# Performance work log

Hardware: AMD Instinct MI355X
Metric: run time of the kernel (lower is better)

The kernel has to match this reference:

```python
import jax, jax.numpy as jnp
import numpy as np

INPUT, HIDDEN, OUTPUT, BATCH = 2048, 32, 512, 16384


def setup_inputs() -> dict:
    key = jax.random.key(0)
    k1, k2, k3, k4 = jax.random.split(key, 4)
    x = jax.random.normal(k1, (BATCH, INPUT), dtype=jnp.float32)
    # torch init: uniform(-1, 1) for both linear weights and hebbian coeffs
    w1 = jax.random.uniform(k2, (HIDDEN, INPUT), jnp.float32, -1.0, 1.0)
    w2 = jax.random.uniform(k3, (OUTPUT, HIDDEN), jnp.float32, -1.0, 1.0)
    heb_coeffs = jax.random.uniform(k4, (HIDDEN * INPUT + OUTPUT * HIDDEN, 4), jnp.float32, -1.0, 1.0)
    return {"x": x, "w1": w1, "w2": w2, "heb_coeffs": heb_coeffs}


def reference(x, w1, w2, heb_coeffs):
    # Forward MLP: act = relu(x @ w1^T), out = sigmoid(act @ w2^T) - 0.4
    act = jax.nn.relu(x @ w1.T)                 # [B, HIDDEN]
    out = jax.nn.sigmoid(act @ w2.T) - 0.4      # [B, OUTPUT]

    B = x.shape[0]
    # idx = (shape0-1)*i + i + j == shape0*i + j  -> coeff layout [in_dim, out_dim, 4]
    c1 = heb_coeffs[: HIDDEN * INPUT].reshape(INPUT, HIDDEN, 4)
    c2 = heb_coeffs[HIDDEN * INPUT :].reshape(HIDDEN, OUTPUT, 4)

    # ABCD update, batch loop -> batch-summed outer products / rank-1 terms
    corr1 = jnp.einsum("bi,bj->ij", x, act)     # [INPUT, HIDDEN]
    dw1T = (B * c1[..., 3]
            + c1[..., 0] * corr1
            + c1[..., 1] * x.sum(0)[:, None]
            + c1[..., 2] * act.sum(0)[None, :])  # [INPUT, HIDDEN]

    corr2 = jnp.einsum("bi,bj->ij", act, out)   # [HIDDEN, OUTPUT]
    dw2T = (B * c2[..., 3]
            + c2[..., 0] * corr2
            + c2[..., 1] * act.sum(0)[:, None]
            + c2[..., 2] * out.sum(0)[None, :])  # [HIDDEN, OUTPUT]

    w1_new = w1 + dw1T.T                        # [HIDDEN, INPUT]
    w2_new = w2 + dw2T.T                        # [OUTPUT, HIDDEN]
    # row-wise L2 normalization (torch.norm(dim=1, keepdim=True))
    w1_new = w1_new / jnp.linalg.norm(w1_new, axis=1, keepdims=True)
    w2_new = w2_new / jnp.linalg.norm(w2_new, axis=1, keepdims=True)
    return out, w1_new, w2_new
```

## Files before the change

### kernel.cpp

```cpp
#include <hip/hip_runtime.h>
#include <math.h>

constexpr int BATCH = 16384;
constexpr int IND   = 2048;
constexpr int HID   = 32;
constexpr int OUTD  = 512;

constexpr int NC1 = 64;
constexpr int NSA = 64;
constexpr int NC2 = 128;

constexpr int SA   = 136;
constexpr int SXT  = 72;
constexpr int SATW = 136;
constexpr int SAT2 = 264;

typedef __attribute__((ext_vector_type(8))) short bf16x8;
typedef __attribute__((ext_vector_type(4))) float f32x4;

__device__ __forceinline__ unsigned short f2bf(float f) {
  unsigned u = __float_as_uint(f);
  u += 0x7FFFu + ((u >> 16) & 1u);
  return (unsigned short)(u >> 16);
}
__device__ __forceinline__ float bf2f(unsigned short h) {
  return __uint_as_float(((unsigned)h) << 16);
}
__device__ __forceinline__ void split2(float f, unsigned short& hi,
                                       unsigned short& lo) {
  hi = f2bf(f);
  lo = f2bf(f - bf2f(hi));
}
__device__ __forceinline__ int swzA(int row, int col) {
  return row * SA + (col ^ (((row >> 3) & 7) * 8));
}

__global__ __launch_bounds__(256) void k_cvtw(
    const float* __restrict__ w1, const float* __restrict__ w2,
    unsigned short* __restrict__ w1H, unsigned short* __restrict__ w1L,
    unsigned short* __restrict__ w2H, unsigned short* __restrict__ w2L) {
  const int bid = blockIdx.x;
  if (bid < 64) {
    const int g = bid * 256 + threadIdx.x;
    float4 v = ((const float4*)w1)[g];
    ushort4 h, l;
    split2(v.x, h.x, l.x); split2(v.y, h.y, l.y);
    split2(v.z, h.z, l.z); split2(v.w, h.w, l.w);
    ((ushort4*)w1H)[g] = h;
    ((ushort4*)w1L)[g] = l;
  } else {
    const int g = (bid - 64) * 256 + threadIdx.x;
    float4 v = ((const float4*)w2)[g];
    ushort4 h, l;
    split2(v.x, h.x, l.x); split2(v.y, h.y, l.y);
    split2(v.z, h.z, l.z); split2(v.w, h.w, l.w);
    ((ushort4*)w2H)[g] = h;
    ((ushort4*)w2L)[g] = l;
  }
}

__global__ __launch_bounds__(256, 4) void k_act(
    const float* __restrict__ x, const unsigned short* __restrict__ w1H,
    const unsigned short* __restrict__ w1L, float* __restrict__ act_part,
    unsigned short* __restrict__ xH) {
  const int tid = threadIdx.x;
  const int kq = blockIdx.x & 1;
  const int bt = blockIdx.x >> 1;
  const int b0 = bt * 32;
  const int kbase = kq * 1024;
  const int lane = tid & 63;
  const int wv = tid >> 6;
  const int arow = lane & 15;
  const int m4 = lane >> 4;
  const int ksub = m4 * 8;
  const int rt = wv & 1;
  const int ht = wv >> 1;

  __shared__ __align__(16) unsigned short XH[32 * SA];
  __shared__ __align__(16) unsigned short XL[32 * SA];
  __shared__ __align__(16) unsigned short WH[32 * SA];
  __shared__ __align__(16) unsigned short WL[32 * SA];

  const int rp = tid >> 4;
  const int kg = (tid & 15) * 8;

  float4 px0a, px0b, px1a, px1b;
  bf16x8 pwh0, pwl0, pwh1, pwl1;

#define LOADA(K0)                                                          \
  {                                                                        \
    const float* xr0 = x + (size_t)(b0 + 2 * rp) * IND + kbase + (K0) + kg;\
    const float* xr1 = xr0 + IND;                                          \
    px0a = *(const float4*)(xr0);                                          \
    px0b = *(const float4*)(xr0 + 4);                                      \
    px1a = *(const float4*)(xr1);                                          \
    px1b = *(const float4*)(xr1 + 4);                                      \
    const size_t wo = (size_t)(2 * rp) * IND + kbase + (K0) + kg;          \
    pwh0 = *(const bf16x8*)(&w1H[wo]);                                     \
    pwl0 = *(const bf16x8*)(&w1L[wo]);                                     \
    pwh1 = *(const bf16x8*)(&w1H[wo + IND]);                               \
    pwl1 = *(const bf16x8*)(&w1L[wo + IND]);                               \
  }

#define PUTX2(ROW, COL, V, GK)                                       \
  {                                                                  \
    ushort4 h_, l_;                                                  \
    split2((V).x, h_.x, l_.x); split2((V).y, h_.y, l_.y);            \
    split2((V).z, h_.z, l_.z); split2((V).w, h_.w, l_.w);            \
    *(ushort4*)(&XH[swzA((ROW), (COL))]) = h_;                       \
    *(ushort4*)(&XL[swzA((ROW), (COL))]) = l_;                       \
    *(ushort4*)(&xH[(size_t)(b0 + (ROW)) * IND + (GK) + (COL)]) = h_;\
  }

#define STOREA(GK)                                                   \
  {                                                                  \
    PUTX2(2 * rp, kg, px0a, GK);                                     \
    PUTX2(2 * rp, kg + 4, px0b, GK);                                 \
    PUTX2(2 * rp + 1, kg, px1a, GK);                                 \
    PUTX2(2 * rp + 1, kg + 4, px1b, GK);                             \
    *(bf16x8*)(&WH[swzA(2 * rp, kg)]) = pwh0;                        \
    *(bf16x8*)(&WL[swzA(2 * rp, kg)]) = pwl0;                        \
    *(bf16x8*)(&WH[swzA(2 * rp + 1, kg)]) = pwh1;                    \
    *(bf16x8*)(&WL[swzA(2 * rp + 1, kg)]) = pwl1;                    \
  }

  f32x4 accA = {0.f, 0.f, 0.f, 0.f};
  LOADA(0);

  for (int kc = 0; kc < 8; ++kc) {
    __syncthreads();
    STOREA(kbase + kc * 128);
    __syncthreads();
    if (kc < 7) LOADA((kc + 1) * 128);
    const int xrow = rt * 16 + arow;
    const int wrow = ht * 16 + arow;
#pragma unroll
    for (int ks = 0; ks < 4; ++ks) {
      const int kk = ks * 32 + ksub;
      bf16x8 ah = *(const bf16x8*)(&XH[swzA(xrow, kk)]);
      bf16x8 al = *(const bf16x8*)(&XL[swzA(xrow, kk)]);
      bf16x8 bh = *(const bf16x8*)(&WH[swzA(wrow, kk)]);
      bf16x8 bl_ = *(const bf16x8*)(&WL[swzA(wrow, kk)]);
      accA = __builtin_amdgcn_mfma_f32_16x16x32_bf16(ah, bh, accA, 0, 0, 0);
      accA = __builtin_amdgcn_mfma_f32_16x16x32_bf16(ah, bl_, accA, 0, 0, 0);
      accA = __builtin_amdgcn_mfma_f32_16x16x32_bf16(al, bh, accA, 0, 0, 0);
    }
  }

  const int bl = rt * 16 + (m4 << 2);
  const int h = ht * 16 + arow;
  float* p = act_part + (size_t)kq * (BATCH * HID);
#pragma unroll
  for (int r = 0; r < 4; ++r)
    p[(size_t)(b0 + bl + r) * HID + h] = accA[r];
}

__global__ __launch_bounds__(256) void k_actc(
    const float* __restrict__ act_part,
    unsigned short* __restrict__ actH, unsigned short* __restrict__ actL,
    unsigned short* __restrict__ actT, float* __restrict__ actsum_part) {
  const int tid = threadIdx.x;
  const int blk = blockIdx.x;
  const int b0 = blk * 256;

  __shared__ unsigned short asT[32][264];
  __shared__ float red[256][4];

  const float4* p0 = (const float4*)act_part;
  const float4* p1 = p0 + (size_t)BATCH * HID / 4;

  const int hq = tid & 7;
  float4 s{0.f, 0.f, 0.f, 0.f};
#pragma unroll
  for (int r = 0; r < 8; ++r) {
    const int e4 = r * 256 + tid;
    const int b = e4 >> 3;
    const size_t g = (size_t)(b0 + b) * 8 + hq;
    float4 a = p0[g];
    float4 c = p1[g];
    a.x = fmaxf(a.x + c.x, 0.f);  a.y = fmaxf(a.y + c.y, 0.f);
    a.z = fmaxf(a.z + c.z, 0.f);  a.w = fmaxf(a.w + c.w, 0.f);
    ushort4 hh, ll;
    split2(a.x, hh.x, ll.x); split2(a.y, hh.y, ll.y);
    split2(a.z, hh.z, ll.z); split2(a.w, hh.w, ll.w);
    *(ushort4*)(&actH[g * 4]) = hh;
    *(ushort4*)(&actL[g * 4]) = ll;
    asT[hq * 4 + 0][b] = hh.x;
    asT[hq * 4 + 1][b] = hh.y;
    asT[hq * 4 + 2][b] = hh.z;
    asT[hq * 4 + 3][b] = hh.w;
    s.x += a.x; s.y += a.y; s.z += a.z; s.w += a.w;
  }
  red[tid][0] = s.x; red[tid][1] = s.y;
  red[tid][2] = s.z; red[tid][3] = s.w;
  __syncthreads();

#pragma unroll
  for (int r = 0; r < 4; ++r) {
    const int slot = r * 256 + tid;
    const int hrow = slot >> 5;
    const int bseg = (slot & 31) * 8;
    bf16x8 v = *(const bf16x8*)(&asT[hrow][bseg]);
    *(bf16x8*)(&actT[(size_t)hrow * BATCH + b0 + bseg]) = v;
  }
  if (tid < 32) {
    const int q = tid >> 2, j = tid & 3;
    float t = 0.f;
#pragma unroll
    for (int sx = 0; sx < 32; ++sx) t += red[q + 8 * sx][j];
    actsum_part[blk * HID + tid] = t;
  }
}

__global__ __launch_bounds__(512, 3) void k_corr1(
    const unsigned short* __restrict__ xH,
    const unsigned short* __restrict__ actT,
    float* __restrict__ corr1T_part, float* __restrict__ xsum_part) {
  const int tid = threadIdx.x;
  const int bc = blockIdx.x >> 4;
  const int iq = blockIdx.x & 15;
  const int b0 = bc * 256;
  const int ibase = iq * 128;
  const int lane = tid & 63;
  const int wv = tid >> 6;
  const int arow = lane & 15;
  const int m4 = lane >> 4;
  const int ksub = m4 * 8;
  const int it = wv * 16;

  __shared__ __align__(16) unsigned short XT[128 * SXT];
  __shared__ __align__(16) unsigned short AT[48 * SAT2];

  for (int e = tid; e < 16 * SAT2; e += 512)
    AT[32 * SAT2 + e] = (unsigned short)0x3F80;
  {
    const int hrow = tid >> 4;
    const int sg = (tid & 15) * 16;
    const int sw = ((hrow >> 3) & 7) * 8;
#pragma unroll
    for (int j = 0; j < 2; ++j) {
      const int boff = sg + 8 * j;
      bf16x8 v = *(const bf16x8*)(&actT[(size_t)hrow * BATCH + b0 + boff]);
      *(bf16x8*)(&AT[hrow * SAT2 + (boff ^ sw)]) = v;
    }
  }

  const int ig = tid & 15;
  const int bq = tid >> 4;

  bf16x8 xa, ya;

#define LOADC(HF)                                                           \
  {                                                                         \
    const int icol = ibase + ig * 8;                                        \
    const unsigned short* r0 =                                              \
        xH + (size_t)(b0 + 64 * (HF) + 2 * bq) * IND + icol;                \
    xa = *(const bf16x8*)(r0);                                              \
    ya = *(const bf16x8*)(r0 + IND);                                        \
  }

#define STC                                                                 \
  {                                                                         \
    const int qb = (2 * bq) ^ ((ig & 7) * 8);                               \
    unsigned short* basew = &XT[(size_t)(ig * 8) * SXT + qb];               \
    ushort2 p;                                                              \
    p.x = (unsigned short)xa[0]; p.y = (unsigned short)ya[0];               \
    *(ushort2*)(basew + 0 * SXT) = p;                                       \
    p.x = (unsigned short)xa[1]; p.y = (unsigned short)ya[1];               \
    *(ushort2*)(basew + 1 * SXT) = p;                                       \
    p.x = (unsigned short)xa[2]; p.y = (unsigned short)ya[2];               \
    *(ushort2*)(basew + 2 * SXT) = p;                                       \
    p.x = (unsigned short)xa[3]; p.y = (unsigned short)ya[3];               \
    *(ushort2*)(basew + 3 * SXT) = p;                                       \
    p.x = (unsigned short)xa[4]; p.y = (unsigned short)ya[4];               \
    *(ushort2*)(basew + 4 * SXT) = p;                                       \
    p.x = (unsigned short)xa[5]; p.y = (unsigned short)ya[5];               \
    *(ushort2*)(basew + 5 * SXT) = p;                                       \
    p.x = (unsigned short)xa[6]; p.y = (unsigned short)ya[6];               \
    *(ushort2*)(basew + 6 * SXT) = p;                                       \
    p.x = (unsigned short)xa[7]; p.y = (unsigned short)ya[7];               \
    *(ushort2*)(basew + 7 * SXT) = p;                                       \
  }

  const int swzr = (((it + arow) >> 3) & 7) * 8;
  const int swze0 = ((arow >> 3) & 7) * 8;
  const int swze1 = (((16 + arow) >> 3) & 7) * 8;

  f32x4 c00 = {0.f, 0.f, 0.f, 0.f};
  f32x4 c01 = {0.f, 0.f, 0.f, 0.f};
  f32x4 c02 = {0.f, 0.f, 0.f, 0.f};

  LOADC(0);
#pragma unroll
  for (int hf = 0; hf < 4; ++hf) {
    __syncthreads();
    STC;
    __syncthreads();
    if (hf < 3) LOADC(hf + 1);
#pragma unroll
    for (int bs = 0; bs < 2; ++bs) {
      const int bb = bs * 32 + ksub;
      const int bb2 = 64 * hf + bb;
      bf16x8 a = *(const bf16x8*)(&XT[(it + arow) * SXT + (bb ^ swzr)]);
      bf16x8 e0 = *(const bf16x8*)(&AT[arow * SAT2 + (bb2 ^ swze0)]);
      bf16x8 e1 = *(const bf16x8*)(&AT[(16 + arow) * SAT2 + (bb2 ^ swze1)]);
      bf16x8 e2 = *(const bf16x8*)(&AT[(32 + arow) * SAT2 + bb2]);
      c00 = __builtin_amdgcn_mfma_f32_16x16x32_bf16(a, e0, c00, 0, 0, 0);
      c01 = __builtin_amdgcn_mfma_f32_16x16x32_bf16(a, e1, c01, 0, 0, 0);
      c02 = __builtin_amdgcn_mfma_f32_16x16x32_bf16(a, e2, c02, 0, 0, 0);
    }
  }

  float* basep = corr1T_part + (size_t)bc * (IND * HID);
  const int gi = ibase + it + (m4 << 2);
  *(f32x4*)(basep + (size_t)arow * IND + gi) = c00;
  *(f32x4*)(basep + (size_t)(16 + arow) * IND + gi) = c01;
  if (arow == 0)
    *(f32x4*)(xsum_part + (size_t)bc * IND + gi) = c02;
}

__global__ __launch_bounds__(256) void k_red1(
    const float* __restrict__ c1p, const float* __restrict__ xsp,
    const float* __restrict__ asp,
    float* __restrict__ corr1T, float* __restrict__ xsum,
    float* __restrict__ actsum) {
  const int e = blockIdx.x * 256 + threadIdx.x;
  float s = 0.f;
#pragma unroll 8
  for (int c = 0; c < NC1; ++c) s += c1p[(size_t)c * (IND * HID) + e];
  corr1T[e] = s;
  if (e < IND) {
    float t = 0.f;
#pragma unroll 8
    for (int c = 0; c < NC1; ++c) t += xsp[(size_t)c * IND + e];
    xsum[e] = t;
  }
  if (e < HID) {
    float t = 0.f;
#pragma unroll 8
    for (int c = 0; c < NSA; ++c) t += asp[(size_t)c * HID + e];
    actsum[e] = t;
  }
}

__global__ __launch_bounds__(256, 2) void k_fwd2m(
    const unsigned short* __restrict__ actH,
    const unsigned short* __restrict__ actL,
    const unsigned short* __restrict__ actT,
    const unsigned short* __restrict__ w2H,
    const unsigned short* __restrict__ w2L,
    float* __restrict__ out, float* __restrict__ corr2_part,
    float* __restrict__ outsum_part) {
  const int tid = threadIdx.x;
  const int bc = blockIdx.x >> 2;
  const int og = blockIdx.x & 3;
  const int b0 = bc * 128;
  const int obase = og * 128;
  const int lane = tid & 63;
  const int wv = tid >> 6;
  const int arow = lane & 15;
  const int m4 = lane >> 4;
  const int ksub = m4 * 8;

  __shared__ __align__(16) unsigned short W2Hs[128 * 40];
  __shared__ __align__(16) unsigned short W2Ls[128 * 40];
  __shared__ __align__(16) unsigned short AH[64 * 40];
  __shared__ __align__(16) unsigned short AL[64 * 40];
  __shared__ __align__(16) unsigned short AT[48 * SATW];
  __shared__ __align__(16) unsigned short OT[128 * 72];

  {
    const int r2 = tid >> 1, hh = (tid & 1) * 16;
    const size_t wo = (size_t)(obase + r2) * HID + hh;
    *(bf16x8*)(&W2Hs[r2 * 40 + hh]) = *(const bf16x8*)(&w2H[wo]);
    *(bf16x8*)(&W2Hs[r2 * 40 + hh + 8]) = *(const bf16x8*)(&w2H[wo + 8]);
    *(bf16x8*)(&W2Ls[r2 * 40 + hh]) = *(const bf16x8*)(&w2L[wo]);
    *(bf16x8*)(&W2Ls[r2 * 40 + hh + 8]) = *(const bf16x8*)(&w2L[wo + 8]);
  }
  {
    const int h = tid >> 3, seg16 = (tid & 7) * 16;
#pragma unroll
    for (int j = 0; j < 2; ++j) {
      const int seg = seg16 + 8 * j;
      *(bf16x8*)(&AT[h * SATW + seg]) =
          *(const bf16x8*)(&actT[(size_t)h * BATCH + b0 + seg]);
    }
  }
  for (int e = tid; e < 16 * SATW; e += 256)
    AT[32 * SATW + e] = (unsigned short)0x3F80;

  f32x4 c0a = {0.f,0.f,0.f,0.f}, c1a = {0.f,0.f,0.f,0.f}, c2a = {0.f,0.f,0.f,0.f};
  f32x4 c0b = {0.f,0.f,0.f,0.f}, c1b = {0.f,0.f,0.f,0.f}, c2b = {0.f,0.f,0.f,0.f};

  for (int hf = 0; hf < 2; ++hf) {
    __syncthreads();
    {
      const int b = tid >> 2, q = (tid & 3) * 8;
      *(bf16x8*)(&AH[b * 40 + q]) =
          *(const bf16x8*)(&actH[(size_t)(b0 + 64 * hf + b) * HID + q]);
      *(bf16x8*)(&AL[b * 40 + q]) =
          *(const bf16x8*)(&actL[(size_t)(b0 + 64 * hf + b) * HID + q]);
    }
    __syncthreads();

    const int bt = wv;
    bf16x8 fah = *(const bf16x8*)(&AH[(bt * 16 + arow) * 40 + ksub]);
    bf16x8 fal = *(const bf16x8*)(&AL[(bt * 16 + arow) * 40 + ksub]);
#pragma unroll
    for (int ot = 0; ot < 8; ++ot) {
      bf16x8 wbh = *(const bf16x8*)(&W2Hs[(ot * 16 + arow) * 40 + ksub]);
      bf16x8 wbl = *(const bf16x8*)(&W2Ls[(ot * 16 + arow) * 40 + ksub]);
      f32x4 z = {0.f, 0.f, 0.f, 0.f};
      z = __builtin_amdgcn_mfma_f32_16x16x32_bf16(fah, wbh, z, 0, 0, 0);
      z = __builtin_amdgcn_mfma_f32_16x16x32_bf16(fah, wbl, z, 0, 0, 0);
      z = __builtin_amdgcn_mfma_f32_16x16x32_bf16(fal, wbh, z, 0, 0, 0);
      ushort4 po;
      {
        float ov0 = 1.0f / (1.0f + __expf(-z[0])) - 0.4f;
        float ov1 = 1.0f / (1.0f + __expf(-z[1])) - 0.4f;
        float ov2 = 1.0f / (1.0f + __expf(-z[2])) - 0.4f;
        float ov3 = 1.0f / (1.0f + __expf(-z[3])) - 0.4f;
        const size_t ob = (size_t)(b0 + 64 * hf + bt * 16 + m4 * 4) * OUTD +
                          obase + ot * 16 + arow;
        out[ob + 0 * OUTD] = ov0;
        out[ob + 1 * OUTD] = ov1;
        out[ob + 2 * OUTD] = ov2;
        out[ob + 3 * OUTD] = ov3;
        po.x = f2bf(ov0); po.y = f2bf(ov1); po.z = f2bf(ov2); po.w = f2bf(ov3);
      }
      *(ushort4*)(&OT[(ot * 16 + arow) * 72 + bt * 16 + m4 * 4]) = po;
    }
    __syncthreads();

    {
      const int ot = wv * 2;
#pragma unroll
      for (int ks = 0; ks < 2; ++ks) {
        const int bb = ks * 32 + ksub;
        const int bb2 = 64 * hf + bb;
        bf16x8 bo = *(const bf16x8*)(&OT[(ot * 16 + arow) * 72 + bb]);
        bf16x8 a0 = *(const bf16x8*)(&AT[arow * SATW + bb2]);
        bf16x8 a1 = *(const bf16x8*)(&AT[(16 + arow) * SATW + bb2]);
        bf16x8 a2 = *(const bf16x8*)(&AT[(32 + arow) * SATW + bb2]);
        c0a = __builtin_amdgcn_mfma_f32_16x16x32_bf16(a0, bo, c0a, 0, 0, 0);
        c1a = __builtin_amdgcn_mfma_f32_16x16x32_bf16(a1, bo, c1a, 0, 0, 0);
        c2a = __builtin_amdgcn_mfma_f32_16x16x32_bf16(a2, bo, c2a, 0, 0, 0);
      }
    }
    {
      const int ot = wv * 2 + 1;
#pragma unroll
      for (int ks = 0; ks < 2; ++ks) {
        const int bb = ks * 32 + ksub;
        const int bb2 = 64 * hf + bb;
        bf16x8 bo = *(const bf16x8*)(&OT[(ot * 16 + arow) * 72 + bb]);
        bf16x8 a0 = *(const bf16x8*)(&AT[arow * SATW + bb2]);
        bf16x8 a1 = *(const bf16x8*)(&AT[(16 + arow) * SATW + bb2]);
        bf16x8 a2 = *(const bf16x8*)(&AT[(32 + arow) * SATW + bb2]);
        c0b = __builtin_amdgcn_mfma_f32_16x16x32_bf16(a0, bo, c0b, 0, 0, 0);
        c1b = __builtin_amdgcn_mfma_f32_16x16x32_bf16(a1, bo, c1b, 0, 0, 0);
        c2b = __builtin_amdgcn_mfma_f32_16x16x32_bf16(a2, bo, c2b, 0, 0, 0);
      }
    }
  }

  {
    const int ot0 = wv * 2, ot1 = wv * 2 + 1;
    float* cp0 = corr2_part + (size_t)bc * (HID * OUTD) + obase + ot0 * 16 + arow;
    float* cp1 = corr2_part + (size_t)bc * (HID * OUTD) + obase + ot1 * 16 + arow;
#pragma unroll
    for (int r = 0; r < 4; ++r) {
      cp0[(size_t)(m4 * 4 + r) * OUTD] = c0a[r];
      cp0[(size_t)(16 + m4 * 4 + r) * OUTD] = c1a[r];
      cp1[(size_t)(m4 * 4 + r) * OUTD] = c0b[r];
      cp1[(size_t)(16 + m4 * 4 + r) * OUTD] = c1b[r];
    }
    if (m4 == 0) {
      outsum_part[(size_t)bc * OUTD + obase + ot0 * 16 + arow] = c2a[0];
      outsum_part[(size_t)bc * OUTD + obase + ot1 * 16 + arow] = c2b[0];
    }
  }
}

__global__ __launch_bounds__(256) void k_red2(
    const float* __restrict__ corr2_part, const float* __restrict__ outsum_part,
    float* __restrict__ corr2, float* __restrict__ outsum) {
  const int e = blockIdx.x * 256 + threadIdx.x;
  float s = 0.f;
#pragma unroll 8
  for (int c = 0; c < NC2; ++c) s += corr2_part[(size_t)c * (HID * OUTD) + e];
  corr2[e] = s;
  if (e < OUTD) {
    float t = 0.f;
#pragma unroll 8
    for (int c = 0; c < NC2; ++c) t += outsum_part[(size_t)c * OUTD + e];
    outsum[e] = t;
  }
}

__global__ __launch_bounds__(256) void k_w1(
    const float* __restrict__ w1, const float* __restrict__ heb,
    const float* __restrict__ corr1T, const float* __restrict__ xsum,
    const float* __restrict__ actsum, float* __restrict__ w1out) {
  const int h = blockIdx.x;
  const int tid = threadIdx.x;
  const float ash = actsum[h];
  const float4* heb4 = (const float4*)heb;

  float val[8];
  float ss = 0.f;
#pragma unroll
  for (int r = 0; r < 8; ++r) {
    const int i = tid + 256 * r;
    float4 c = heb4[(size_t)i * HID + h];
    float v = w1[(size_t)h * IND + i] + 16384.0f * c.w +
              c.x * corr1T[(size_t)h * IND + i] + c.y * xsum[i] + c.z * ash;
    val[r] = v;
    ss += v * v;
  }

  __shared__ float red[256];
  red[tid] = ss;
  __syncthreads();
  for (int s = 128; s > 0; s >>= 1) {
    if (tid < s) red[tid] += red[tid + s];
    __syncthreads();
  }
  const float inv = 1.0f / sqrtf(red[0]);
#pragma unroll
  for (int r = 0; r < 8; ++r) {
    const int i = tid + 256 * r;
    w1out[(size_t)h * IND + i] = val[r] * inv;
  }
}

__global__ __launch_bounds__(256) void k_w2(
    const float* __restrict__ w2, const float* __restrict__ heb,
    const float* __restrict__ corr2, const float* __restrict__ actsum,
    const float* __restrict__ outsum, float* __restrict__ w2out) {
  const int o = blockIdx.x * 256 + threadIdx.x;
  const float oso = outsum[o];
  const float4* heb4 = (const float4*)heb;

  float val[HID];
  float ss = 0.f;
#pragma unroll
  for (int h = 0; h < HID; ++h) {
    float4 c = heb4[(size_t)(HID * IND) + (size_t)h * OUTD + o];
    float v = w2[(size_t)o * HID + h] + 16384.0f * c.w +
              c.x * corr2[(size_t)h * OUTD + o] + c.y * actsum[h] + c.z * oso;
    val[h] = v;
    ss += v * v;
  }
  const float inv = 1.0f / sqrtf(ss);
#pragma unroll
  for (int h = 0; h < HID; ++h) w2out[(size_t)o * HID + h] = val[h] * inv;
}

extern "C" void kernel_launch(void* const* d_in, const int* in_sizes, int n_in,
                              void* d_out, int out_size, void* d_ws,
                              size_t ws_size, hipStream_t stream) {
  const float* x   = (const float*)d_in[0];
  const float* w1  = (const float*)d_in[1];
  const float* w2  = (const float*)d_in[2];
  const float* heb = (const float*)d_in[3];

  float* out = (float*)d_out;
  float* w1o = out + (size_t)BATCH * OUTD;
  float* w2o = w1o + (size_t)HID * IND;

  float* ws = (float*)d_ws;
  unsigned short* actH = (unsigned short*)ws;
  unsigned short* actL = actH + (size_t)BATCH * HID;
  unsigned short* actT = actL + (size_t)BATCH * HID;
  unsigned short* w1H  = actT + (size_t)BATCH * HID;
  unsigned short* w1L  = w1H + (size_t)HID * IND;
  unsigned short* w2H  = w1L + (size_t)HID * IND;
  unsigned short* w2L  = w2H + (size_t)OUTD * HID;
  unsigned short* xH   = w2L + (size_t)OUTD * HID;
  float* corr1T      = (float*)(xH + (size_t)BATCH * IND);
  float* corr2       = corr1T + (size_t)IND * HID;
  float* xsum        = corr2 + (size_t)HID * OUTD;
  float* actsum      = xsum + IND;
  float* outsum      = actsum + HID;
  float* act_part    = outsum + OUTD;
  float* corr1T_part = act_part + (size_t)2 * BATCH * HID;
  float* xsum_part   = corr1T_part + (size_t)NC1 * IND * HID;
  float* actsum_part = xsum_part + (size_t)NC1 * IND;
  float* corr2_part  = actsum_part + (size_t)NSA * HID;
  float* outsum_part = corr2_part + (size_t)NC2 * HID * OUTD;

  k_cvtw <<<80, 256, 0, stream>>>(w1, w2, w1H, w1L, w2H, w2L);
  k_act  <<<1024, 256, 0, stream>>>(x, w1H, w1L, act_part, xH);
  k_actc <<<64, 256, 0, stream>>>(act_part, actH, actL, actT, actsum_part);
  k_corr1<<<1024, 512, 0, stream>>>(xH, actT, corr1T_part, xsum_part);
  k_red1 <<<256, 256, 0, stream>>>(corr1T_part, xsum_part, actsum_part,
                                   corr1T, xsum, actsum);
  k_fwd2m<<<512, 256, 0, stream>>>(actH, actL, actT, w2H, w2L, out,
                                   corr2_part, outsum_part);
  k_red2 <<<64, 256, 0, stream>>>(corr2_part, outsum_part, corr2, outsum);
  k_w1   <<<32, 256, 0, stream>>>(w1, heb, corr1T, xsum, actsum, w1o);
  k_w2   <<<2, 256, 0, stream>>>(w2, heb, corr2, actsum, outsum, w2o);
}
```

Before: 116.3 us.

## Fuse act finalize into k_act by dropping the K-split

k_act no longer splits K across two blocks. Each block now covers the full 2048 reduction and applies the relu itself. It then writes actH/actL/actT and the per-block act sums directly, which removes the k_actc kernel and the act_part round trip through global memory. The cost is half as many blocks (512) with twice the serial K loop each, less parallelism, and scattered 2-byte stores for actH/actL. k_red1 must now reduce 512 actsum partials instead of 64.

```diff
diff --git a/kernel.cpp b/kernel.cpp
--- a/kernel.cpp
+++ b/kernel.cpp
@@ -7,7 +7,7 @@
 constexpr int OUTD  = 512;
 
 constexpr int NC1 = 64;
-constexpr int NSA = 64;
+constexpr int NSA = 512;
 constexpr int NC2 = 128;
 
 constexpr int SA   = 136;
@@ -61,13 +61,12 @@
 
 __global__ __launch_bounds__(256, 4) void k_act(
     const float* __restrict__ x, const unsigned short* __restrict__ w1H,
-    const unsigned short* __restrict__ w1L, float* __restrict__ act_part,
-    unsigned short* __restrict__ xH) {
+    const unsigned short* __restrict__ w1L, unsigned short* __restrict__ xH,
+    unsigned short* __restrict__ actH, unsigned short* __restrict__ actL,
+    unsigned short* __restrict__ actT, float* __restrict__ actsum_part) {
   const int tid = threadIdx.x;
-  const int kq = blockIdx.x & 1;
-  const int bt = blockIdx.x >> 1;
+  const int bt = blockIdx.x;
   const int b0 = bt * 32;
-  const int kbase = kq * 1024;
   const int lane = tid & 63;
   const int wv = tid >> 6;
   const int arow = lane & 15;
@@ -76,10 +75,11 @@
   const int rt = wv & 1;
   const int ht = wv >> 1;
 
-  __shared__ __align__(16) unsigned short XH[32 * SA];
-  __shared__ __align__(16) unsigned short XL[32 * SA];
-  __shared__ __align__(16) unsigned short WH[32 * SA];
-  __shared__ __align__(16) unsigned short WL[32 * SA];
+  __shared__ __align__(16) unsigned short XHs[32 * SA];
+  __shared__ __align__(16) unsigned short XLs[32 * SA];
+  __shared__ __align__(16) unsigned short WHs[32 * SA];
+  __shared__ __align__(16) unsigned short WLs[32 * SA];
+  __shared__ float asum_s[32][8];
 
   const int rp = tid >> 4;
   const int kg = (tid & 15) * 8;
@@ -89,13 +89,13 @@
 
 #define LOADA(K0)                                                          \
   {                                                                        \
-    const float* xr0 = x + (size_t)(b0 + 2 * rp) * IND + kbase + (K0) + kg;\
+    const float* xr0 = x + (size_t)(b0 + 2 * rp) * IND + (K0) + kg;        \
     const float* xr1 = xr0 + IND;                                          \
     px0a = *(const float4*)(xr0);                                          \
     px0b = *(const float4*)(xr0 + 4);                                      \
     px1a = *(const float4*)(xr1);                                          \
     px1b = *(const float4*)(xr1 + 4);                                      \
-    const size_t wo = (size_t)(2 * rp) * IND + kbase + (K0) + kg;          \
+    const size_t wo = (size_t)(2 * rp) * IND + (K0) + kg;                  \
     pwh0 = *(const bf16x8*)(&w1H[wo]);                                     \
     pwl0 = *(const bf16x8*)(&w1L[wo]);                                     \
     pwh1 = *(const bf16x8*)(&w1H[wo + IND]);                               \
@@ -107,8 +107,8 @@
     ushort4 h_, l_;                                                  \
     split2((V).x, h_.x, l_.x); split2((V).y, h_.y, l_.y);            \
     split2((V).z, h_.z, l_.z); split2((V).w, h_.w, l_.w);            \
-    *(ushort4*)(&XH[swzA((ROW), (COL))]) = h_;                       \
-    *(ushort4*)(&XL[swzA((ROW), (COL))]) = l_;                       \
+    *(ushort4*)(&XHs[swzA((ROW), (COL))]) = h_;                      \
+    *(ushort4*)(&XLs[swzA((ROW), (COL))]) = l_;                      \
     *(ushort4*)(&xH[(size_t)(b0 + (ROW)) * IND + (GK) + (COL)]) = h_;\
   }
 
@@ -118,97 +118,64 @@
     PUTX2(2 * rp, kg + 4, px0b, GK);                                 \
     PUTX2(2 * rp + 1, kg, px1a, GK);                                 \
     PUTX2(2 * rp + 1, kg + 4, px1b, GK);                             \
-    *(bf16x8*)(&WH[swzA(2 * rp, kg)]) = pwh0;                        \
-    *(bf16x8*)(&WL[swzA(2 * rp, kg)]) = pwl0;                        \
-    *(bf16x8*)(&WH[swzA(2 * rp + 1, kg)]) = pwh1;                    \
-    *(bf16x8*)(&WL[swzA(2 * rp + 1, kg)]) = pwl1;                    \
+    *(bf16x8*)(&WHs[swzA(2 * rp, kg)]) = pwh0;                       \
+    *(bf16x8*)(&WLs[swzA(2 * rp, kg)]) = pwl0;                       \
+    *(bf16x8*)(&WHs[swzA(2 * rp + 1, kg)]) = pwh1;                   \
+    *(bf16x8*)(&WLs[swzA(2 * rp + 1, kg)]) = pwl1;                   \
   }
 
   f32x4 accA = {0.f, 0.f, 0.f, 0.f};
   LOADA(0);
 
-  for (int kc = 0; kc < 8; ++kc) {
-    __syncthreads();
-    STOREA(kbase + kc * 128);
-    __syncthreads();
-    if (kc < 7) LOADA((kc + 1) * 128);
+  for (int kc = 0; kc < 16; ++kc) {
+    __syncthreads();
+    STOREA(kc * 128);
+    __syncthreads();
+    if (kc < 15) LOADA((kc + 1) * 128);
     const int xrow = rt * 16 + arow;
     const int wrow = ht * 16 + arow;
 #pragma unroll
     for (int ks = 0; ks < 4; ++ks) {
       const int kk = ks * 32 + ksub;
-      bf16x8 ah = *(const bf16x8*)(&XH[swzA(xrow, kk)]);
-      bf16x8 al = *(const bf16x8*)(&XL[swzA(xrow, kk)]);
-      bf16x8 bh = *(const bf16x8*)(&WH[swzA(wrow, kk)]);
-      bf16x8 bl_ = *(const bf16x8*)(&WL[swzA(wrow, kk)]);
+      bf16x8 ah = *(const bf16x8*)(&XHs[swzA(xrow, kk)]);
+      bf16x8 al = *(const bf16x8*)(&XLs[swzA(xrow, kk)]);
+      bf16x8 bh = *(const bf16x8*)(&WHs[swzA(wrow, kk)]);
+      bf16x8 bl_ = *(const bf16x8*)(&WLs[swzA(wrow, kk)]);
       accA = __builtin_amdgcn_mfma_f32_16x16x32_bf16(ah, bh, accA, 0, 0, 0);
       accA = __builtin_amdgcn_mfma_f32_16x16x32_bf16(ah, bl_, accA, 0, 0, 0);
       accA = __builtin_amdgcn_mfma_f32_16x16x32_bf16(al, bh, accA, 0, 0, 0);
     }
   }
 
+#pragma unroll
+  for (int r = 0; r < 4; ++r) accA[r] = fmaxf(accA[r], 0.f);
+
   const int bl = rt * 16 + (m4 << 2);
   const int h = ht * 16 + arow;
-  float* p = act_part + (size_t)kq * (BATCH * HID);
-#pragma unroll
-  for (int r = 0; r < 4; ++r)
-    p[(size_t)(b0 + bl + r) * HID + h] = accA[r];
-}
-
-__global__ __launch_bounds__(256) void k_actc(
-    const float* __restrict__ act_part,
-    unsigned short* __restrict__ actH, unsigned short* __restrict__ actL,
-    unsigned short* __restrict__ actT, float* __restrict__ actsum_part) {
-  const int tid = threadIdx.x;
-  const int blk = blockIdx.x;
-  const int b0 = blk * 256;
-
-  __shared__ unsigned short asT[32][264];
-  __shared__ float red[256][4];
-
-  const float4* p0 = (const float4*)act_part;
-  const float4* p1 = p0 + (size_t)BATCH * HID / 4;
-
-  const int hq = tid & 7;
-  float4 s{0.f, 0.f, 0.f, 0.f};
-#pragma unroll
-  for (int r = 0; r < 8; ++r) {
-    const int e4 = r * 256 + tid;
-    const int b = e4 >> 3;
-    const size_t g = (size_t)(b0 + b) * 8 + hq;
-    float4 a = p0[g];
-    float4 c = p1[g];
-    a.x = fmaxf(a.x + c.x, 0.f);  a.y = fmaxf(a.y + c.y, 0.f);
-    a.z = fmaxf(a.z + c.z, 0.f);  a.w = fmaxf(a.w + c.w, 0.f);
-    ushort4 hh, ll;
-    split2(a.x, hh.x, ll.x); split2(a.y, hh.y, ll.y);
-    split2(a.z, hh.z, ll.z); split2(a.w, hh.w, ll.w);
-    *(ushort4*)(&actH[g * 4]) = hh;
-    *(ushort4*)(&actL[g * 4]) = ll;
-    asT[hq * 4 + 0][b] = hh.x;
-    asT[hq * 4 + 1][b] = hh.y;
-    asT[hq * 4 + 2][b] = hh.z;
-    asT[hq * 4 + 3][b] = hh.w;
-    s.x += a.x; s.y += a.y; s.z += a.z; s.w += a.w;
-  }
-  red[tid][0] = s.x; red[tid][1] = s.y;
-  red[tid][2] = s.z; red[tid][3] = s.w;
+  ushort4 hh4, ll4;
+  {
+    unsigned short h0_, l0_, h1_, l1_, h2_, l2_, h3_, l3_;
+    split2(accA[0], h0_, l0_);
+    split2(accA[1], h1_, l1_);
+    split2(accA[2], h2_, l2_);
+    split2(accA[3], h3_, l3_);
+    hh4.x = h0_; hh4.y = h1_; hh4.z = h2_; hh4.w = h3_;
+    ll4.x = l0_; ll4.y = l1_; ll4.z = l2_; ll4.w = l3_;
+  }
+#pragma unroll
+  for (int r = 0; r < 4; ++r) {
+    actH[(size_t)(b0 + bl + r) * HID + h] = (&hh4.x)[r];
+    actL[(size_t)(b0 + bl + r) * HID + h] = (&ll4.x)[r];
+  }
+  *(ushort4*)(&actT[(size_t)h * BATCH + b0 + bl]) = hh4;
+
+  asum_s[h][rt * 4 + m4] = accA[0] + accA[1] + accA[2] + accA[3];
   __syncthreads();
-
-#pragma unroll
-  for (int r = 0; r < 4; ++r) {
-    const int slot = r * 256 + tid;
-    const int hrow = slot >> 5;
-    const int bseg = (slot & 31) * 8;
-    bf16x8 v = *(const bf16x8*)(&asT[hrow][bseg]);
-    *(bf16x8*)(&actT[(size_t)hrow * BATCH + b0 + bseg]) = v;
-  }
   if (tid < 32) {
-    const int q = tid >> 2, j = tid & 3;
-    float t = 0.f;
-#pragma unroll
-    for (int sx = 0; sx < 32; ++sx) t += red[q + 8 * sx][j];
-    actsum_part[blk * HID + tid] = t;
+    float s = 0.f;
+#pragma unroll
+    for (int q = 0; q < 8; ++q) s += asum_s[tid][q];
+    actsum_part[bt * HID + tid] = s;
   }
 }
 
@@ -583,16 +550,15 @@
   float* xsum        = corr2 + (size_t)HID * OUTD;
   float* actsum      = xsum + IND;
   float* outsum      = actsum + HID;
-  float* act_part    = outsum + OUTD;
-  float* corr1T_part = act_part + (size_t)2 * BATCH * HID;
+  float* corr1T_part = outsum + OUTD;
   float* xsum_part   = corr1T_part + (size_t)NC1 * IND * HID;
   float* actsum_part = xsum_part + (size_t)NC1 * IND;
   float* corr2_part  = actsum_part + (size_t)NSA * HID;
   float* outsum_part = corr2_part + (size_t)NC2 * HID * OUTD;
 
   k_cvtw <<<80, 256, 0, stream>>>(w1, w2, w1H, w1L, w2H, w2L);
-  k_act  <<<1024, 256, 0, stream>>>(x, w1H, w1L, act_part, xH);
-  k_actc <<<64, 256, 0, stream>>>(act_part, actH, actL, actT, actsum_part);
+  k_act  <<<512, 256, 0, stream>>>(x, w1H, w1L, xH, actH, actL, actT,
+                                   actsum_part);
   k_corr1<<<1024, 512, 0, stream>>>(xH, actT, corr1T_part, xsum_part);
   k_red1 <<<256, 256, 0, stream>>>(corr1T_part, xsum_part, actsum_part,
                                    corr1T, xsum, actsum);
```

Result: slower. 140.7 us (+20.9%).
